# Performance work log

Measured on AMD Instinct MI355X. Metric: run time of the kernel, lower is better.

The kernel has to match this reference:

```python
import jax, jax.numpy as jnp
import numpy as np


def setup_inputs() -> dict:
    key0 = jax.random.key(0)
    kq, kk, kv = jax.random.split(key0, 3)
    B, S, H, KVH, D = 1, 4096, 8, 2, 64
    return {
        "query": jax.random.normal(kq, (B, S, H, D), dtype=jnp.float32),
        "key": jax.random.normal(kk, (B, S, KVH, D), dtype=jnp.float32),
        "value": jax.random.normal(kv, (B, S, KVH, D), dtype=jnp.float32),
    }


def _ring_attn_single(query, key, value):
    # world_size == 1 (dist uninitialized): ring loop is a single local step
    # with query_offset == key_offset == 0.
    B, S, H, D = query.shape
    KVH = key.shape[2]
    scale = D ** -0.5
    # [B, H, S, D]
    q = query.transpose(0, 2, 1, 3)
    k = key.transpose(0, 2, 1, 3)
    v = value.transpose(0, 2, 1, 3)
    if KVH != H:
        rep = H // KVH
        k = jnp.repeat(k, rep, axis=1)  # repeat_interleave on head dim
        v = jnp.repeat(v, rep, axis=1)
    logits = jnp.einsum("bhqd,bhkd->bhqk", q, k) * scale
    pos = jnp.arange(S)
    causal = pos[:, None] < pos[None, :]  # mask future keys
    logits = jnp.where(causal[None, None], -jnp.inf, logits)
    w = jax.nn.softmax(logits, axis=-1)  # [B, H, S, S]
    attn_out = jnp.einsum("bhqk,bhkd->bhqd", w, v)
    cw = jnp.sum(w, axis=-1, keepdims=True)  # chunk softmax mass (== 1)
    out = attn_out * cw / (cw + 1e-8)  # weight-accumulation renorm
    return out.transpose(0, 2, 1, 3)  # [B, S, H, D]


def reference(query, key, value):
    return _ring_attn_single(query, key, value)
```

## Files before the change

### kernel.cpp

```cpp
#include <hip/hip_runtime.h>
#include <hip/hip_bf16.h>


#define S_LEN 4096
#define H_Q   8
#define H_KV  2
#define DH    64
#define BM    64
#define BN    64
#define PITCH 72
#define NEG_BIG (-1e30f)
#define CS (0.125f * 1.44269504088896340736f)

#define NT_SPLIT 160
#define SLOTS    (NT_SPLIT * H_Q)
#define KB_SH    (S_LEN * H_KV * DH)
#define OB_FLOATS ((size_t)SLOTS * BM * DH)
#define WS_NEED  ((size_t)(2 * KB_SH) * 2 + (OB_FLOATS + (size_t)SLOTS * BM) * 4)

typedef __attribute__((ext_vector_type(8))) short bf16x8;
typedef __attribute__((ext_vector_type(4))) float f32x4;

__device__ __forceinline__ short bf(float x) {
    return __builtin_bit_cast(short, __float2bfloat16(x));
}

__global__ __launch_bounds__(256)
void ring_attn_prepass(const float* __restrict__ K, const float* __restrict__ V,
                       short* __restrict__ Kb, short* __restrict__ Vt) {
    const int b = blockIdx.x;
    const int t = threadIdx.x;
    if (b < 512) {
        const int i = (b * 256 + t) * 4;
        float4 kv = *(const float4*)(K + i);
        unsigned int p0 = (unsigned int)(unsigned short)bf(kv.x)
                        | ((unsigned int)(unsigned short)bf(kv.y) << 16);
        unsigned int p1 = (unsigned int)(unsigned short)bf(kv.z)
                        | ((unsigned int)(unsigned short)bf(kv.w) << 16);
        *(unsigned int*)(Kb + i)     = p0;
        *(unsigned int*)(Kb + i + 2) = p1;
    } else {
        __shared__ short T[DH * PITCH];
        const int bb  = b - 512;
        const int kvh = bb >> 6;
        const int s0  = (bb & 63) * 64;
        {
            const int r  = t >> 2;
            const int dq = (t & 3) * 16;
            const float* vp = V + ((s0 + r) * H_KV + kvh) * DH + dq;
            float4 a0 = *(const float4*)(vp);
            float4 a1 = *(const float4*)(vp + 4);
            float4 a2 = *(const float4*)(vp + 8);
            float4 a3 = *(const float4*)(vp + 12);
            float e[16] = {a0.x,a0.y,a0.z,a0.w, a1.x,a1.y,a1.z,a1.w,
                           a2.x,a2.y,a2.z,a2.w, a3.x,a3.y,a3.z,a3.w};
#pragma unroll
            for (int i = 0; i < 16; ++i)
                T[(dq + i) * PITCH + r] = bf(e[i]);
        }
        __syncthreads();
        {
            const int d  = t >> 2;
            const int sq = (t & 3) * 16;
            bf16x8 x0 = *(const bf16x8*)(&T[d * PITCH + sq]);
            bf16x8 x1 = *(const bf16x8*)(&T[d * PITCH + sq + 8]);
            short* op = Vt + (kvh * DH + d) * S_LEN + s0 + sq;
            *(bf16x8*)(op)     = x0;
            *(bf16x8*)(op + 8) = x1;
        }
    }
}

template <bool SPLIT>
__global__ __launch_bounds__(256)
void ring_attn_fwd(const float* __restrict__ Q, const short* __restrict__ Kb,
                   const short* __restrict__ Vt, float* __restrict__ O,
                   float* __restrict__ Obuf, float* __restrict__ Lbuf) {
    const int bid = blockIdx.x;
    const int h   = bid & 7;
    int qt, nch, jbeg, jend, tr;
    if (SPLIT) {
        tr = (NT_SPLIT - 1) - (bid >> 3);
        int ch;
        if (tr < 16)      { qt = tr;                 ch = 0;              nch = 1; }
        else if (tr < 48) { qt = 16 + (tr - 16) / 2; ch = (tr - 16) % 2; nch = 2; }
        else if (tr < 96) { qt = 32 + (tr - 48) / 3; ch = (tr - 48) % 3; nch = 3; }
        else              { qt = 48 + (tr - 96) / 4; ch = (tr - 96) % 4; nch = 4; }
        jbeg = ch * 16;
        jend = min(qt + 1, jbeg + 16);
    } else {
        tr = 0; qt = (S_LEN / BM - 1) - (bid >> 3);
        nch = 1; jbeg = 0; jend = qt + 1;
    }
    const int kvh = h >> 2;

    __shared__ short Ks[BN * PITCH];
    __shared__ short Vs[DH * PITCH];
    __shared__ short Pw[4][16 * PITCH];

    const int tid  = threadIdx.x;
    const int w    = tid >> 6;
    const int lane = tid & 63;
    const int c    = lane & 15;
    const int q    = lane >> 4;

    bf16x8 qf0, qf1;
    {
        const int qg = qt * BM + w * 16 + c;
        const float* qp = Q + (qg * H_Q + h) * DH + q * 8;
        float4 a0 = *(const float4*)(qp);
        float4 a1 = *(const float4*)(qp + 4);
        float4 b0 = *(const float4*)(qp + 32);
        float4 b1 = *(const float4*)(qp + 36);
        qf0 = bf16x8{bf(a0.x*CS), bf(a0.y*CS), bf(a0.z*CS), bf(a0.w*CS),
                     bf(a1.x*CS), bf(a1.y*CS), bf(a1.z*CS), bf(a1.w*CS)};
        qf1 = bf16x8{bf(b0.x*CS), bf(b0.y*CS), bf(b0.z*CS), bf(b0.w*CS),
                     bf(b1.x*CS), bf(b1.y*CS), bf(b1.z*CS), bf(b1.w*CS)};
    }

    f32x4 acc[4] = {f32x4{0,0,0,0}, f32x4{0,0,0,0}, f32x4{0,0,0,0}, f32x4{0,0,0,0}};
    float l_lane[4] = {0.f, 0.f, 0.f, 0.f};

    const int rr = tid >> 3;
    const int cc = (tid & 7) * 8;

    for (int j = jbeg; j < jend; ++j) {
        __syncthreads();

#pragma unroll
        for (int p = 0; p < 2; ++p) {
            const int n = p * 32 + rr;
            bf16x8 x = *(const bf16x8*)(Kb + ((j * BN + n) * H_KV + kvh) * DH + cc);
            *(bf16x8*)(&Ks[n * PITCH + cc]) = x;
        }
#pragma unroll
        for (int p = 0; p < 2; ++p) {
            const int d = p * 32 + rr;
            bf16x8 x = *(const bf16x8*)(Vt + (kvh * DH + d) * S_LEN + j * BN + cc);
            *(bf16x8*)(&Vs[d * PITCH + cc]) = x;
        }
        __syncthreads();

        f32x4 s[4] = {f32x4{0,0,0,0}, f32x4{0,0,0,0}, f32x4{0,0,0,0}, f32x4{0,0,0,0}};
#pragma unroll
        for (int nt = 0; nt < 4; ++nt) {
            bf16x8 kf0 = *(const bf16x8*)(&Ks[(nt * 16 + c) * PITCH + q * 8]);
            bf16x8 kf1 = *(const bf16x8*)(&Ks[(nt * 16 + c) * PITCH + q * 8 + 32]);
            s[nt] = __builtin_amdgcn_mfma_f32_16x16x32_bf16(qf0, kf0, s[nt], 0, 0, 0);
            s[nt] = __builtin_amdgcn_mfma_f32_16x16x32_bf16(qf1, kf1, s[nt], 0, 0, 0);
        }

        if (j == qt) {
            const int qrow = w * 16 + q * 4;
#pragma unroll
            for (int nt = 0; nt < 4; ++nt) {
                const int kcol = nt * 16 + c;
#pragma unroll
                for (int r = 0; r < 4; ++r)
                    if (kcol > qrow + r) s[nt][r] = NEG_BIG;
            }
        }

#pragma unroll
        for (int nt = 0; nt < 4; ++nt)
#pragma unroll
            for (int r = 0; r < 4; ++r) {
                const float p = exp2f(s[nt][r]);
                s[nt][r] = p;
                l_lane[r] += p;
            }

#pragma unroll
        for (int nt = 0; nt < 4; ++nt)
#pragma unroll
            for (int r = 0; r < 4; ++r)
                Pw[w][(q * 4 + r) * PITCH + nt * 16 + c] = bf(s[nt][r]);

        bf16x8 pf0 = *(const bf16x8*)(&Pw[w][c * PITCH + q * 8]);
        bf16x8 pf1 = *(const bf16x8*)(&Pw[w][c * PITCH + q * 8 + 32]);

#pragma unroll
        for (int dt = 0; dt < 4; ++dt) {
            bf16x8 vf0 = *(const bf16x8*)(&Vs[(dt * 16 + c) * PITCH + q * 8]);
            bf16x8 vf1 = *(const bf16x8*)(&Vs[(dt * 16 + c) * PITCH + q * 8 + 32]);
            acc[dt] = __builtin_amdgcn_mfma_f32_16x16x32_bf16(pf0, vf0, acc[dt], 0, 0, 0);
            acc[dt] = __builtin_amdgcn_mfma_f32_16x16x32_bf16(pf1, vf1, acc[dt], 0, 0, 0);
        }
    }

#pragma unroll
    for (int r = 0; r < 4; ++r) {
        float t2 = l_lane[r];
        t2 += __shfl_xor(t2, 1);
        t2 += __shfl_xor(t2, 2);
        t2 += __shfl_xor(t2, 4);
        t2 += __shfl_xor(t2, 8);
        l_lane[r] = t2;
    }

    if (!SPLIT || nch == 1) {
        const int qg = qt * BM + w * 16;
#pragma unroll
        for (int r = 0; r < 4; ++r) {
            const float inv = 1.0f / l_lane[r];
            const int row = qg + q * 4 + r;
            float* op = O + (row * H_Q + h) * DH + c;
#pragma unroll
            for (int dt = 0; dt < 4; ++dt)
                op[dt * 16] = acc[dt][r] * inv;
        }
    } else {
        const int slot = tr * 8 + h;
        float* ob = Obuf + (size_t)slot * (BM * DH);
#pragma unroll
        for (int r = 0; r < 4; ++r) {
            const int rin = w * 16 + q * 4 + r;
#pragma unroll
            for (int dt = 0; dt < 4; ++dt)
                ob[rin * DH + dt * 16 + c] = acc[dt][r];
            if (c == 0)
                Lbuf[slot * BM + rin] = l_lane[r];
        }
    }
}

__global__ __launch_bounds__(256)
void ring_attn_combine(const float* __restrict__ Obuf, const float* __restrict__ Lbuf,
                       float* __restrict__ O) {
    const int gid  = blockIdx.x * 256 + threadIdx.x;
    const int d    = gid & 63;
    const int h    = (gid >> 6) & 7;
    const int srow = 1024 + (gid >> 9);
    const int qt   = srow >> 6;
    const int rin  = srow & 63;
    int nch, tr0;
    if (qt < 32)      { nch = 2; tr0 = 16 + (qt - 16) * 2; }
    else if (qt < 48) { nch = 3; tr0 = 48 + (qt - 32) * 3; }
    else              { nch = 4; tr0 = 96 + (qt - 48) * 4; }

    float num = 0.0f, den = 0.0f;
    for (int ch = 0; ch < nch; ++ch) {
        const int slot = (tr0 + ch) * 8 + h;
        den += Lbuf[slot * BM + rin];
        num += Obuf[(size_t)slot * (BM * DH) + rin * DH + d];
    }
    O[(srow * H_Q + h) * DH + d] = num / den;
}

extern "C" void kernel_launch(void* const* d_in, const int* in_sizes, int n_in,
                              void* d_out, int out_size, void* d_ws, size_t ws_size,
                              hipStream_t stream) {
    const float* Q = (const float*)d_in[0];
    const float* K = (const float*)d_in[1];
    const float* V = (const float*)d_in[2];
    float* O  = (float*)d_out;
    short* Kb = (short*)d_ws;
    short* Vt = Kb + KB_SH;
    float* Obuf = (float*)(Vt + KB_SH);
    float* Lbuf = Obuf + OB_FLOATS;

    ring_attn_prepass<<<640, 256, 0, stream>>>(K, V, Kb, Vt);
    if (ws_size >= WS_NEED) {
        ring_attn_fwd<true><<<NT_SPLIT * H_Q, 256, 0, stream>>>(Q, Kb, Vt, O, Obuf, Lbuf);
        ring_attn_combine<<<(S_LEN - 1024) * H_Q * DH / 256, 256, 0, stream>>>(Obuf, Lbuf, O);
    } else {
        ring_attn_fwd<false><<<(S_LEN / BM) * H_Q, 256, 0, stream>>>(Q, Kb, Vt, O, Obuf, Lbuf);
    }
}
```

Baseline: 125.3 us.

## Fuse split-K combine into attention kernel via atomic last-block reduction

Removes the separate combine kernel. Each split block now bumps an atomic counter per (q-tile, head), and the last block to finish reduces the partial outputs and sums and writes O. The KV split changes from 16-tile chunks to 12-tile chunks, giving 204 row-tiles instead of 160. The QK MFMA swaps its operands so the score layout feeds straight into the PV MFMA as register A-fragments, which drops the LDS round-trip for P. This saves a launch and shared-memory traffic, at the cost of extra threadfences, an atomic per block, and a serialized tail reduction inside the last block.

```diff
diff --git a/kernel.cpp b/kernel.cpp
--- a/kernel.cpp
+++ b/kernel.cpp
@@ -12,34 +12,38 @@
 #define NEG_BIG (-1e30f)
 #define CS (0.125f * 1.44269504088896340736f)
 
-#define NT_SPLIT 160
-#define SLOTS    (NT_SPLIT * H_Q)
-#define KB_SH    (S_LEN * H_KV * DH)
-#define OB_FLOATS ((size_t)SLOTS * BM * DH)
-#define WS_NEED  ((size_t)(2 * KB_SH) * 2 + (OB_FLOATS + (size_t)SLOTS * BM) * 4)
+#define CHUNK 12
+#define NTR   204
+#define KB_SH (S_LEN * H_KV * DH)
+#define OB_FLOATS ((size_t)NTR * H_Q * BM * DH)
+#define L_FLOATS  ((size_t)NTR * H_Q * BM)
+#define WS_NEED ((size_t)(2 * KB_SH) * 2 + (OB_FLOATS + L_FLOATS) * 4 + 512 * 4)
 
 typedef __attribute__((ext_vector_type(8))) short bf16x8;
+typedef __attribute__((ext_vector_type(4))) short s16x4;
 typedef __attribute__((ext_vector_type(4))) float f32x4;
+typedef __attribute__((ext_vector_type(4))) unsigned int u32x4;
 
 __device__ __forceinline__ short bf(float x) {
     return __builtin_bit_cast(short, __float2bfloat16(x));
 }
+__device__ __forceinline__ unsigned int pk2(float lo, float hi) {
+    return (unsigned int)(unsigned short)bf(lo)
+         | ((unsigned int)(unsigned short)bf(hi) << 16);
+}
 
 __global__ __launch_bounds__(256)
 void ring_attn_prepass(const float* __restrict__ K, const float* __restrict__ V,
-                       short* __restrict__ Kb, short* __restrict__ Vt) {
+                       short* __restrict__ Kb, short* __restrict__ Vt,
+                       int* __restrict__ cnt) {
     const int b = blockIdx.x;
     const int t = threadIdx.x;
     if (b < 512) {
         const int i = (b * 256 + t) * 4;
         float4 kv = *(const float4*)(K + i);
-        unsigned int p0 = (unsigned int)(unsigned short)bf(kv.x)
-                        | ((unsigned int)(unsigned short)bf(kv.y) << 16);
-        unsigned int p1 = (unsigned int)(unsigned short)bf(kv.z)
-                        | ((unsigned int)(unsigned short)bf(kv.w) << 16);
-        *(unsigned int*)(Kb + i)     = p0;
-        *(unsigned int*)(Kb + i + 2) = p1;
-    } else {
+        *(unsigned int*)(Kb + i)     = pk2(kv.x, kv.y);
+        *(unsigned int*)(Kb + i + 2) = pk2(kv.z, kv.w);
+    } else if (b < 640) {
         __shared__ short T[DH * PITCH];
         const int bb  = b - 512;
         const int kvh = bb >> 6;
@@ -68,6 +72,9 @@
             *(bf16x8*)(op)     = x0;
             *(bf16x8*)(op + 8) = x1;
         }
+    } else {
+        cnt[t] = 0;
+        cnt[t + 256] = 0;
     }
 }
 
@@ -75,28 +82,37 @@
 __global__ __launch_bounds__(256)
 void ring_attn_fwd(const float* __restrict__ Q, const short* __restrict__ Kb,
                    const short* __restrict__ Vt, float* __restrict__ O,
-                   float* __restrict__ Obuf, float* __restrict__ Lbuf) {
+                   float* __restrict__ Obuf, float* __restrict__ Lbuf,
+                   int* __restrict__ cnt) {
     const int bid = blockIdx.x;
     const int h   = bid & 7;
-    int qt, nch, jbeg, jend, tr;
+    int qt, nch, jbeg, jend, tr0;
     if (SPLIT) {
-        tr = (NT_SPLIT - 1) - (bid >> 3);
-        int ch;
-        if (tr < 16)      { qt = tr;                 ch = 0;              nch = 1; }
-        else if (tr < 48) { qt = 16 + (tr - 16) / 2; ch = (tr - 16) % 2; nch = 2; }
-        else if (tr < 96) { qt = 32 + (tr - 48) / 3; ch = (tr - 48) % 3; nch = 3; }
-        else              { qt = 48 + (tr - 96) / 4; ch = (tr - 96) % 4; nch = 4; }
-        jbeg = ch * 16;
-        jend = min(qt + 1, jbeg + 16);
-    } else {
-        tr = 0; qt = (S_LEN / BM - 1) - (bid >> 3);
-        nch = 1; jbeg = 0; jend = qt + 1;
+        const int tr = (NTR - 1) - (bid >> 3);
+        int b, base;
+        if (tr < 12)       { b = 0; base = 0; }
+        else if (tr < 36)  { b = 1; base = 12; }
+        else if (tr < 72)  { b = 2; base = 36; }
+        else if (tr < 120) { b = 3; base = 72; }
+        else if (tr < 180) { b = 4; base = 120; }
+        else               { b = 5; base = 180; }
+        const int u  = tr - base;
+        const int qq = u / (b + 1);
+        const int ch = u - qq * (b + 1);
+        qt   = 12 * b + qq;
+        nch  = b + 1;
+        tr0  = base + qq * (b + 1);
+        jbeg = ch * CHUNK;
+        jend = min(qt + 1, jbeg + CHUNK);
+    } else {
+        qt = (S_LEN / BM - 1) - (bid >> 3);
+        nch = 1; jbeg = 0; jend = qt + 1; tr0 = 0;
     }
     const int kvh = h >> 2;
 
     __shared__ short Ks[BN * PITCH];
     __shared__ short Vs[DH * PITCH];
-    __shared__ short Pw[4][16 * PITCH];
+    __shared__ int   sh_last;
 
     const int tid  = threadIdx.x;
     const int w    = tid >> 6;
@@ -119,14 +135,13 @@
     }
 
     f32x4 acc[4] = {f32x4{0,0,0,0}, f32x4{0,0,0,0}, f32x4{0,0,0,0}, f32x4{0,0,0,0}};
-    float l_lane[4] = {0.f, 0.f, 0.f, 0.f};
+    float l_lane = 0.0f;
 
     const int rr = tid >> 3;
     const int cc = (tid & 7) * 8;
 
     for (int j = jbeg; j < jend; ++j) {
         __syncthreads();
-
 #pragma unroll
         for (int p = 0; p < 2; ++p) {
             const int n = p * 32 + rr;
@@ -146,18 +161,18 @@
         for (int nt = 0; nt < 4; ++nt) {
             bf16x8 kf0 = *(const bf16x8*)(&Ks[(nt * 16 + c) * PITCH + q * 8]);
             bf16x8 kf1 = *(const bf16x8*)(&Ks[(nt * 16 + c) * PITCH + q * 8 + 32]);
-            s[nt] = __builtin_amdgcn_mfma_f32_16x16x32_bf16(qf0, kf0, s[nt], 0, 0, 0);
-            s[nt] = __builtin_amdgcn_mfma_f32_16x16x32_bf16(qf1, kf1, s[nt], 0, 0, 0);
+            s[nt] = __builtin_amdgcn_mfma_f32_16x16x32_bf16(kf0, qf0, s[nt], 0, 0, 0);
+            s[nt] = __builtin_amdgcn_mfma_f32_16x16x32_bf16(kf1, qf1, s[nt], 0, 0, 0);
         }
 
         if (j == qt) {
-            const int qrow = w * 16 + q * 4;
+            const int qrl = w * 16 + c;
 #pragma unroll
             for (int nt = 0; nt < 4; ++nt) {
-                const int kcol = nt * 16 + c;
+                const int kl = nt * 16 + q * 4;
 #pragma unroll
                 for (int r = 0; r < 4; ++r)
-                    if (kcol > qrow + r) s[nt][r] = NEG_BIG;
+                    if (kl + r > qrl) s[nt][r] = NEG_BIG;
             }
         }
 
@@ -167,50 +182,51 @@
             for (int r = 0; r < 4; ++r) {
                 const float p = exp2f(s[nt][r]);
                 s[nt][r] = p;
-                l_lane[r] += p;
-            }
-
-#pragma unroll
-        for (int nt = 0; nt < 4; ++nt)
-#pragma unroll
-            for (int r = 0; r < 4; ++r)
-                Pw[w][(q * 4 + r) * PITCH + nt * 16 + c] = bf(s[nt][r]);
-
-        bf16x8 pf0 = *(const bf16x8*)(&Pw[w][c * PITCH + q * 8]);
-        bf16x8 pf1 = *(const bf16x8*)(&Pw[w][c * PITCH + q * 8 + 32]);
+                l_lane += p;
+            }
+
+        u32x4 w0 = {pk2(s[0][0], s[0][1]), pk2(s[0][2], s[0][3]),
+                    pk2(s[1][0], s[1][1]), pk2(s[1][2], s[1][3])};
+        u32x4 w1 = {pk2(s[2][0], s[2][1]), pk2(s[2][2], s[2][3]),
+                    pk2(s[3][0], s[3][1]), pk2(s[3][2], s[3][3])};
+        bf16x8 pf0 = __builtin_bit_cast(bf16x8, w0);
+        bf16x8 pf1 = __builtin_bit_cast(bf16x8, w1);
 
 #pragma unroll
         for (int dt = 0; dt < 4; ++dt) {
-            bf16x8 vf0 = *(const bf16x8*)(&Vs[(dt * 16 + c) * PITCH + q * 8]);
-            bf16x8 vf1 = *(const bf16x8*)(&Vs[(dt * 16 + c) * PITCH + q * 8 + 32]);
+            const int base = (dt * 16 + c) * PITCH;
+            s16x4 v0 = *(const s16x4*)(&Vs[base + 4 * q]);
+            s16x4 v1 = *(const s16x4*)(&Vs[base + 16 + 4 * q]);
+            s16x4 v2 = *(const s16x4*)(&Vs[base + 32 + 4 * q]);
+            s16x4 v3 = *(const s16x4*)(&Vs[base + 48 + 4 * q]);
+            bf16x8 vf0 = bf16x8{v0[0],v0[1],v0[2],v0[3], v1[0],v1[1],v1[2],v1[3]};
+            bf16x8 vf1 = bf16x8{v2[0],v2[1],v2[2],v2[3], v3[0],v3[1],v3[2],v3[3]};
             acc[dt] = __builtin_amdgcn_mfma_f32_16x16x32_bf16(pf0, vf0, acc[dt], 0, 0, 0);
             acc[dt] = __builtin_amdgcn_mfma_f32_16x16x32_bf16(pf1, vf1, acc[dt], 0, 0, 0);
         }
     }
 
-#pragma unroll
-    for (int r = 0; r < 4; ++r) {
-        float t2 = l_lane[r];
-        t2 += __shfl_xor(t2, 1);
-        t2 += __shfl_xor(t2, 2);
-        t2 += __shfl_xor(t2, 4);
-        t2 += __shfl_xor(t2, 8);
-        l_lane[r] = t2;
-    }
+    float t2 = l_lane;
+    t2 += __shfl_xor(t2, 16);
+    t2 += __shfl_xor(t2, 32);
+    float lr[4];
+#pragma unroll
+    for (int r = 0; r < 4; ++r)
+        lr[r] = __shfl(t2, q * 4 + r);
 
     if (!SPLIT || nch == 1) {
         const int qg = qt * BM + w * 16;
 #pragma unroll
         for (int r = 0; r < 4; ++r) {
-            const float inv = 1.0f / l_lane[r];
-            const int row = qg + q * 4 + r;
-            float* op = O + (row * H_Q + h) * DH + c;
+            const float inv = 1.0f / lr[r];
+            float* op = O + ((qg + q * 4 + r) * H_Q + h) * DH + c;
 #pragma unroll
             for (int dt = 0; dt < 4; ++dt)
                 op[dt * 16] = acc[dt][r] * inv;
         }
     } else {
-        const int slot = tr * 8 + h;
+        const int tr_self = tr0 + (jbeg / CHUNK);
+        const int slot = tr_self * 8 + h;
         float* ob = Obuf + (size_t)slot * (BM * DH);
 #pragma unroll
         for (int r = 0; r < 4; ++r) {
@@ -218,33 +234,44 @@
 #pragma unroll
             for (int dt = 0; dt < 4; ++dt)
                 ob[rin * DH + dt * 16 + c] = acc[dt][r];
-            if (c == 0)
-                Lbuf[slot * BM + rin] = l_lane[r];
-        }
-    }
-}
-
-__global__ __launch_bounds__(256)
-void ring_attn_combine(const float* __restrict__ Obuf, const float* __restrict__ Lbuf,
-                       float* __restrict__ O) {
-    const int gid  = blockIdx.x * 256 + threadIdx.x;
-    const int d    = gid & 63;
-    const int h    = (gid >> 6) & 7;
-    const int srow = 1024 + (gid >> 9);
-    const int qt   = srow >> 6;
-    const int rin  = srow & 63;
-    int nch, tr0;
-    if (qt < 32)      { nch = 2; tr0 = 16 + (qt - 16) * 2; }
-    else if (qt < 48) { nch = 3; tr0 = 48 + (qt - 32) * 3; }
-    else              { nch = 4; tr0 = 96 + (qt - 48) * 4; }
-
-    float num = 0.0f, den = 0.0f;
-    for (int ch = 0; ch < nch; ++ch) {
-        const int slot = (tr0 + ch) * 8 + h;
-        den += Lbuf[slot * BM + rin];
-        num += Obuf[(size_t)slot * (BM * DH) + rin * DH + d];
-    }
-    O[(srow * H_Q + h) * DH + d] = num / den;
+        }
+        if (lane < 16)
+            Lbuf[slot * BM + w * 16 + lane] = t2;
+
+        __threadfence();
+        __syncthreads();
+        if (tid == 0) {
+            int old = atomicAdd(&cnt[qt * 8 + h], 1);
+            sh_last = (old == nch - 1);
+        }
+        __syncthreads();
+        if (sh_last) {
+            __threadfence();
+            const int rin = tid >> 2;
+            const int d0  = (tid & 3) * 16;
+            float den = 0.0f;
+            for (int c2 = 0; c2 < nch; ++c2)
+                den += Lbuf[((tr0 + c2) * 8 + h) * BM + rin];
+            float4 num[4] = {};
+            for (int c2 = 0; c2 < nch; ++c2) {
+                const float* ob2 = Obuf + (size_t)((tr0 + c2) * 8 + h) * (BM * DH)
+                                 + rin * DH + d0;
+#pragma unroll
+                for (int i = 0; i < 4; ++i) {
+                    float4 v = *(const float4*)(ob2 + i * 4);
+                    num[i].x += v.x; num[i].y += v.y;
+                    num[i].z += v.z; num[i].w += v.w;
+                }
+            }
+            const float inv = 1.0f / den;
+            float* op = O + ((qt * BM + rin) * H_Q + h) * DH + d0;
+#pragma unroll
+            for (int i = 0; i < 4; ++i) {
+                float4 v = num[i];
+                ((float4*)op)[i] = float4{v.x*inv, v.y*inv, v.z*inv, v.w*inv};
+            }
+        }
+    }
 }
 
 extern "C" void kernel_launch(void* const* d_in, const int* in_sizes, int n_in,
@@ -258,12 +285,12 @@
     short* Vt = Kb + KB_SH;
     float* Obuf = (float*)(Vt + KB_SH);
     float* Lbuf = Obuf + OB_FLOATS;
-
-    ring_attn_prepass<<<640, 256, 0, stream>>>(K, V, Kb, Vt);
+    int*   cnt  = (int*)(Lbuf + L_FLOATS);
+
+    ring_attn_prepass<<<641, 256, 0, stream>>>(K, V, Kb, Vt, cnt);
     if (ws_size >= WS_NEED) {
-        ring_attn_fwd<true><<<NT_SPLIT * H_Q, 256, 0, stream>>>(Q, Kb, Vt, O, Obuf, Lbuf);
-        ring_attn_combine<<<(S_LEN - 1024) * H_Q * DH / 256, 256, 0, stream>>>(Obuf, Lbuf, O);
-    } else {
-        ring_attn_fwd<false><<<(S_LEN / BM) * H_Q, 256, 0, stream>>>(Q, Kb, Vt, O, Obuf, Lbuf);
-    }
-}
+        ring_attn_fwd<true><<<NTR * H_Q, 256, 0, stream>>>(Q, Kb, Vt, O, Obuf, Lbuf, cnt);
+    } else {
+        ring_attn_fwd<false><<<(S_LEN / BM) * H_Q, 256, 0, stream>>>(Q, Kb, Vt, O, Obuf, Lbuf, cnt);
+    }
+}
```

Result: slower. 340.5 us (+171.6%).
